# Performance work log

Measured on AMD Instinct MI355X. Metric: run time of the kernel, lower is better.

Reference implementation:

```python
import jax, jax.numpy as jnp
import numpy as np

N_HEAD, D_MODEL, D_K, D_V = 16, 1024, 64, 64
B, L = 8, 1024
LN_EPS = 1e-5
NEG_INF = -1e9


def setup_inputs() -> dict:
    key = jax.random.key(0)
    ks = jax.random.split(key, 12)
    s = 0.02
    return {
        "q": jax.random.normal(ks[0], (B, L, D_MODEL), jnp.float32),
        "k": jax.random.normal(ks[1], (B, L, D_MODEL), jnp.float32),
        "v": jax.random.normal(ks[2], (B, L, D_MODEL), jnp.float32),
        "mask": jnp.zeros((B, L, L), dtype=bool),
        "wq": jax.random.normal(ks[3], (D_MODEL, N_HEAD * D_K), jnp.float32) * s,
        "bq": jnp.zeros((N_HEAD * D_K,), jnp.float32),
        "wk": jax.random.normal(ks[4], (D_MODEL, N_HEAD * D_K), jnp.float32) * s,
        "bk": jnp.zeros((N_HEAD * D_K,), jnp.float32),
        "wv": jax.random.normal(ks[5], (D_MODEL, N_HEAD * D_V), jnp.float32) * s,
        "bv": jnp.zeros((N_HEAD * D_V,), jnp.float32),
        "wo": jax.random.normal(ks[6], (N_HEAD * D_V, D_MODEL), jnp.float32) * s,
        "bo": jnp.zeros((D_MODEL,), jnp.float32),
        "gamma": jnp.ones((D_MODEL,), jnp.float32),
        "beta": jnp.zeros((D_MODEL,), jnp.float32),
    }


def reference(q, k, v, mask, wq, bq, wk, bk, wv, bv, wo, bo, gamma, beta):
    b, lq, _ = q.shape
    lk = k.shape[1]
    residual = q
    # separate Q/K/V projections, split heads: [b, len, h, d]
    qh = (q @ wq + bq).reshape(b, lq, N_HEAD, D_K)
    kh = (k @ wk + bk).reshape(b, lk, N_HEAD, D_K)
    vh = (v @ wv + bv).reshape(b, lk, N_HEAD, D_V)
    # scaled dot-product attention (temperature = sqrt(d_k))
    scores = jnp.einsum("bqhd,bkhd->bhqk", qh, kh) / jnp.sqrt(jnp.float32(D_K))
    scores = jnp.where(mask[:, None, :, :], NEG_INF, scores)
    attn = jax.nn.softmax(scores, axis=-1)  # [b, h, lq, lk]
    ctx = jnp.einsum("bhqk,bkhd->bqhd", attn, vh).reshape(b, lq, N_HEAD * D_V)
    # out-proj (dropout is identity in eval) + residual + LayerNorm
    out = ctx @ wo + bo + residual
    mu = out.mean(-1, keepdims=True)
    var = out.var(-1, keepdims=True)
    out = (out - mu) * jax.lax.rsqrt(var + LN_EPS) * gamma + beta
    # match original attn layout: [n_head*b, lq, lk]
    attn_flat = attn.transpose(1, 0, 2, 3).reshape(N_HEAD * b, lq, lk)
    return out, attn_flat
```

## Files before the change

kernel.cpp:

```cpp
#include <hip/hip_runtime.h>
#include <stdint.h>

static constexpr int BATCH  = 8;
static constexpr int SEQ    = 1024;
static constexpr int DMODEL = 1024;
static constexpr int NHEAD  = 16;

typedef __attribute__((ext_vector_type(8))) short sh8;
typedef __attribute__((ext_vector_type(4))) float fl4;

__device__ __forceinline__ uint16_t f2bf(float f) {
    union { float f; uint32_t u; } a; a.f = f;
    uint32_t r = a.u + 0x7FFFu + ((a.u >> 16) & 1u);
    return (uint16_t)(r >> 16);
}

__device__ __forceinline__ float b2f(uint16_t u) {
    union { uint32_t u; float f; } a; a.u = ((uint32_t)u) << 16; return a.f;
}

__device__ __forceinline__ uint32_t cvtpk(float lo, float hi) {
    uint32_t r;
    asm("v_cvt_pk_bf16_f32 %0, %1, %2" : "=v"(r) : "v"(lo), "v"(hi));
    return r;
}

__device__ __forceinline__ sh8 pack_bf8(fl4 x0, fl4 x1) {
    union { uint32_t w[4]; sh8 v; } pk;
    pk.w[0] = cvtpk(x0[0], x0[1]); pk.w[1] = cvtpk(x0[2], x0[3]);
    pk.w[2] = cvtpk(x1[0], x1[1]); pk.w[3] = cvtpk(x1[2], x1[3]);
    return pk.v;
}

__device__ __forceinline__ fl4 mfma16(sh8 a, sh8 b, fl4 c) {
    return __builtin_amdgcn_mfma_f32_16x16x32_bf16(a, b, c, 0, 0, 0);
}

__device__ __forceinline__ void gload16(const void* g, void* l) {
    __builtin_amdgcn_global_load_lds(
        (const __attribute__((address_space(1))) void*)g,
        (__attribute__((address_space(3))) void*)l, 16, 0, 0);
}

__global__ __launch_bounds__(256) void prep_kernel(const float* __restrict__ wq, const float* __restrict__ wk,
                                                   const float* __restrict__ wv, const float* __restrict__ wo,
                                                   uint16_t* __restrict__ tq, uint16_t* __restrict__ tk,
                                                   uint16_t* __restrict__ tv, uint16_t* __restrict__ to) {
    __shared__ uint16_t T[64][72];
    const int z = blockIdx.z;
    const int tid = threadIdx.x;
    const float* w = (z == 0) ? wq : (z == 1) ? wk : (z == 2) ? wv : wo;
    uint16_t* wT = (z == 0) ? tq : (z == 1) ? tk : (z == 2) ? tv : to;
    const float ws = (z == 0) ? 0.125f : 1.f;
    const int n0 = blockIdx.x * 64, k0 = blockIdx.y * 64;
    #pragma unroll
    for (int it = 0; it < 4; ++it) {
        int g = it * 256 + tid;
        int r = g >> 4, c = (g & 15) * 4;
        fl4 x = *(const fl4*)(w + (size_t)(k0 + r) * DMODEL + n0 + c);
        T[r][c + 0] = f2bf(x[0] * ws); T[r][c + 1] = f2bf(x[1] * ws);
        T[r][c + 2] = f2bf(x[2] * ws); T[r][c + 3] = f2bf(x[3] * ws);
    }
    __syncthreads();
    #pragma unroll
    for (int it = 0; it < 4; ++it) {
        int g = it * 256 + tid;
        int r = g >> 4, c = (g & 15) * 4;
        ushort4 o;
        o.x = T[c + 0][r]; o.y = T[c + 1][r]; o.z = T[c + 2][r]; o.w = T[c + 3][r];
        *(ushort4*)(wT + (size_t)(n0 + r) * DMODEL + k0 + c) = o;
    }
}

__global__ __launch_bounds__(256)
void gemm_proj(const float* __restrict__ q, const float* __restrict__ k, const float* __restrict__ v,
               const uint16_t* __restrict__ B0, const uint16_t* __restrict__ B1, const uint16_t* __restrict__ B2,
               const float* __restrict__ b0, const float* __restrict__ b1, const float* __restrict__ b2,
               uint16_t* __restrict__ qh, uint16_t* __restrict__ kh, uint16_t* __restrict__ vT) {
    __shared__ uint16_t lds[128 * 128];
    uint16_t* Alds = lds;
    uint16_t* Blds = lds + 128 * 64;
    const int z = blockIdx.z;
    const float* Af    = (z == 0) ? q : (z == 1) ? k : v;
    const uint16_t* Bt = (z == 0) ? B0 : (z == 1) ? B1 : B2;
    const float* bias  = (z == 0) ? b0 : (z == 1) ? b1 : b2;
    const float bs     = (z == 0) ? 0.125f : 1.f;
    const int m0 = blockIdx.x * 128, n0 = blockIdx.y * 128;
    const int tid = threadIdx.x, lane = tid & 63, wid = tid >> 6;
    const int wr = (wid >> 1) * 64, wc = (wid & 1) * 64;
    const int fr = lane & 15, fk = (lane >> 4) * 8, frow4 = (lane >> 4) * 4;

    fl4 acc[4][4];
    #pragma unroll
    for (int i = 0; i < 4; ++i)
        #pragma unroll
        for (int j = 0; j < 4; ++j) acc[i][j] = (fl4){0.f, 0.f, 0.f, 0.f};

    for (int kt = 0; kt < 16; ++kt) {
        const int kb = kt * 64;
        #pragma unroll
        for (int it = 0; it < 4; ++it) {
            const int g = it * 256 + tid;
            const int r = g >> 3, c = (g & 7) << 3;
            const float* p = Af + (size_t)(m0 + r) * DMODEL + kb + c;
            fl4 x0 = *(const fl4*)p, x1 = *(const fl4*)(p + 4);
            *(sh8*)&Alds[r * 64 + c] = pack_bf8(x0, x1);
            const int lofs = __builtin_amdgcn_readfirstlane((it * 256 + wid * 64) * 16);
            gload16(Bt + (size_t)(n0 + r) * DMODEL + kb + c, (char*)Blds + lofs);
        }
        __syncthreads();
        #pragma unroll
        for (int ks = 0; ks < 2; ++ks) {
            sh8 a[4], bb[4];
            #pragma unroll
            for (int mi = 0; mi < 4; ++mi) a[mi] = *(const sh8*)&Alds[(wr + mi * 16 + fr) * 64 + ks * 32 + fk];
            #pragma unroll
            for (int ni = 0; ni < 4; ++ni) bb[ni] = *(const sh8*)&Blds[(wc + ni * 16 + fr) * 64 + ks * 32 + fk];
            #pragma unroll
            for (int mi = 0; mi < 4; ++mi)
                #pragma unroll
                for (int ni = 0; ni < 4; ++ni) acc[mi][ni] = mfma16(a[mi], bb[ni], acc[mi][ni]);
        }
        __syncthreads();
    }

    if (z < 2) {
        #pragma unroll
        for (int mi = 0; mi < 4; ++mi) {
            #pragma unroll
            for (int ni = 0; ni < 4; ++ni) {
                const int col = wc + ni * 16 + fr;
                const float bv = bias[n0 + col] * bs;
                #pragma unroll
                for (int i = 0; i < 4; ++i) {
                    const int row = wr + mi * 16 + frow4 + i;
                    lds[row * 128 + ((((col >> 3) ^ (row & 7)) << 3) | (col & 7))] = f2bf(acc[mi][ni][i] + bv);
                }
            }
        }
        __syncthreads();
        uint16_t* Cv = (z == 0) ? qh : kh;
        #pragma unroll
        for (int it = 0; it < 8; ++it) {
            const int ch = it * 256 + tid;
            const int row = ch >> 4, cc = ch & 15;
            sh8 vv = *(sh8*)&lds[row * 128 + ((cc ^ (row & 7)) << 3)];
            *(sh8*)(Cv + (size_t)(m0 + row) * DMODEL + n0 + cc * 8) = vv;
        }
    } else {
        #pragma unroll
        for (int mi = 0; mi < 4; ++mi) {
            #pragma unroll
            for (int ni = 0; ni < 4; ++ni) {
                const int col = wc + ni * 16 + fr;
                const float bv = bias[n0 + col];
                #pragma unroll
                for (int i = 0; i < 4; ++i) {
                    const int row = wr + mi * 16 + frow4 + i;
                    lds[col * 128 + ((((row >> 3) ^ (col & 7)) << 3) | (row & 7))] = f2bf(acc[mi][ni][i] + bv);
                }
            }
        }
        __syncthreads();
        const int b = m0 >> 10, l0 = m0 & 1023;
        #pragma unroll
        for (int it = 0; it < 8; ++it) {
            const int ch = it * 256 + tid;
            const int col = ch >> 4, rc = ch & 15;
            sh8 vv = *(sh8*)&lds[col * 128 + ((rc ^ (col & 7)) << 3)];
            *(sh8*)(vT + (size_t)(b * 1024 + n0 + col) * SEQ + l0 + rc * 8) = vv;
        }
    }
}

__global__ __launch_bounds__(256)
void gemm_out(const uint16_t* __restrict__ Ab, const uint16_t* __restrict__ Bt,
              const float* __restrict__ bias, const float* __restrict__ resid,
              float* __restrict__ Cv) {
    __shared__ uint16_t lds[128 * 128];
    uint16_t* Alds = lds;
    uint16_t* Blds = lds + 128 * 64;
    const int m0 = blockIdx.x * 128, n0 = blockIdx.y * 128;
    const int tid = threadIdx.x, lane = tid & 63, wid = tid >> 6;
    const int wr = (wid >> 1) * 64, wc = (wid & 1) * 64;
    const int fr = lane & 15, fk = (lane >> 4) * 8, frow4 = (lane >> 4) * 4;

    fl4 acc[4][4];
    #pragma unroll
    for (int i = 0; i < 4; ++i)
        #pragma unroll
        for (int j = 0; j < 4; ++j) acc[i][j] = (fl4){0.f, 0.f, 0.f, 0.f};

    for (int kt = 0; kt < 16; ++kt) {
        const int kb = kt * 64;
        #pragma unroll
        for (int it = 0; it < 4; ++it) {
            const int g = it * 256 + tid;
            const int r = g >> 3, c = (g & 7) << 3;
            const int lofs = __builtin_amdgcn_readfirstlane((it * 256 + wid * 64) * 16);
            gload16(Ab + (size_t)(m0 + r) * DMODEL + kb + c, (char*)Alds + lofs);
            gload16(Bt + (size_t)(n0 + r) * DMODEL + kb + c, (char*)Blds + lofs);
        }
        __syncthreads();
        #pragma unroll
        for (int ks = 0; ks < 2; ++ks) {
            sh8 a[4], bb[4];
            #pragma unroll
            for (int mi = 0; mi < 4; ++mi) a[mi] = *(const sh8*)&Alds[(wr + mi * 16 + fr) * 64 + ks * 32 + fk];
            #pragma unroll
            for (int ni = 0; ni < 4; ++ni) bb[ni] = *(const sh8*)&Blds[(wc + ni * 16 + fr) * 64 + ks * 32 + fk];
            #pragma unroll
            for (int mi = 0; mi < 4; ++mi)
                #pragma unroll
                for (int ni = 0; ni < 4; ++ni) acc[mi][ni] = mfma16(a[mi], bb[ni], acc[mi][ni]);
        }
        __syncthreads();
    }

    float* flds = (float*)lds;
    #pragma unroll
    for (int h2 = 0; h2 < 2; ++h2) {
        if (h2) __syncthreads();
        if (wc == h2 * 64) {
            #pragma unroll
            for (int ni = 0; ni < 4; ++ni) {
                const int col = wc + ni * 16 + fr;
                const int ch = col - h2 * 64;
                const float bv = bias[n0 + col];
                #pragma unroll
                for (int mi = 0; mi < 4; ++mi) {
                    #pragma unroll
                    for (int i = 0; i < 4; ++i) {
                        const int row = wr + mi * 16 + frow4 + i;
                        float val = acc[mi][ni][i] + bv;
                        val += resid[(size_t)(m0 + row) * DMODEL + n0 + col];
                        flds[row * 64 + ((((ch >> 2) ^ (row & 7)) << 2) | (ch & 3))] = val;
                    }
                }
            }
        }
        __syncthreads();
        #pragma unroll
        for (int it = 0; it < 8; ++it) {
            const int ck = it * 256 + tid;
            const int row = ck >> 4, cc = ck & 15;
            fl4 vv = *(fl4*)&flds[row * 64 + ((cc ^ (row & 7)) << 2)];
            *(fl4*)(Cv + (size_t)(m0 + row) * DMODEL + n0 + h2 * 64 + cc * 4) = vv;
        }
    }
}

__global__ __launch_bounds__(256)
void attn_kernel(const uint16_t* __restrict__ qh, const uint16_t* __restrict__ kh,
                 const uint16_t* __restrict__ vT, const uint8_t* __restrict__ mask,
                 float* __restrict__ attn, uint16_t* __restrict__ ctx) {
    __shared__ uint16_t S[16 * 1024];
    __shared__ float rinv[16];
    const int b = blockIdx.x, h = blockIdx.y, q0 = blockIdx.z * 16;
    const int tid = threadIdx.x, lane = tid & 63, wid = tid >> 6;
    const int fr = lane & 15, fk = (lane >> 4) * 8, frow4 = (lane >> 4) * 4;

    sh8 Aq[2];
    #pragma unroll
    for (int ks = 0; ks < 2; ++ks)
        Aq[ks] = *(const sh8*)(qh + (size_t)(b * SEQ + q0 + fr) * DMODEL + h * 64 + ks * 32 + fk);

    for (int t8 = 0; t8 < 8; ++t8) {
        const int kv0 = (t8 * 4 + wid) * 32;
        sh8 Bk[2][2];
        #pragma unroll
        for (int ni = 0; ni < 2; ++ni)
            #pragma unroll
            for (int ks = 0; ks < 2; ++ks)
                Bk[ni][ks] = *(const sh8*)(kh + (size_t)(b * SEQ + kv0 + ni * 16 + fr) * DMODEL + h * 64 + ks * 32 + fk);
        fl4 sa[2];
        #pragma unroll
        for (int ni = 0; ni < 2; ++ni) sa[ni] = (fl4){0.f, 0.f, 0.f, 0.f};
        #pragma unroll
        for (int ni = 0; ni < 2; ++ni)
            #pragma unroll
            for (int ks = 0; ks < 2; ++ks) sa[ni] = mfma16(Aq[ks], Bk[ni][ks], sa[ni]);
        #pragma unroll
        for (int ni = 0; ni < 2; ++ni)
            #pragma unroll
            for (int i = 0; i < 4; ++i) {
                const int row = frow4 + i, col = kv0 + ni * 16 + fr;
                S[row * 1024 + ((((col >> 3) ^ (row & 15)) << 3) | (col & 7))] = f2bf(sa[ni][i]);
            }
    }
    __syncthreads();

    {
        const int r = tid >> 4, j = tid & 15;
        const int rbase = r * 1024;
        const uint8_t* mbase = mask + (size_t)(b * SEQ + q0 + r) * SEQ;
        sh8 x[8];
        uint2 mw[8];
        #pragma unroll
        for (int c4 = 0; c4 < 8; ++c4) {
            const int cc = c4 * 16 + j;
            x[c4] = *(sh8*)&S[rbase + ((cc ^ r) << 3)];
            mw[c4] = *(const uint2*)(mbase + cc * 8);
        }
        uint32_t anym = 0;
        #pragma unroll
        for (int c4 = 0; c4 < 8; ++c4) anym |= (mw[c4].x | mw[c4].y);
        float mx = -1e30f;
        if (anym == 0) {
            #pragma unroll
            for (int c4 = 0; c4 < 8; ++c4)
                #pragma unroll
                for (int t = 0; t < 8; ++t) mx = fmaxf(mx, b2f((uint16_t)x[c4][t]));
        } else {
            #pragma unroll
            for (int c4 = 0; c4 < 8; ++c4) {
                float f[8];
                #pragma unroll
                for (int t = 0; t < 4; ++t)
                    f[t] = ((mw[c4].x >> (t * 8)) & 0xFF) ? -1e9f : b2f((uint16_t)x[c4][t]);
                #pragma unroll
                for (int t = 0; t < 4; ++t)
                    f[4 + t] = ((mw[c4].y >> (t * 8)) & 0xFF) ? -1e9f : b2f((uint16_t)x[c4][4 + t]);
                union { uint32_t w[4]; sh8 v; } pk;
                pk.w[0] = cvtpk(f[0], f[1]); pk.w[1] = cvtpk(f[2], f[3]);
                pk.w[2] = cvtpk(f[4], f[5]); pk.w[3] = cvtpk(f[6], f[7]);
                x[c4] = pk.v;
                #pragma unroll
                for (int t = 0; t < 8; ++t) mx = fmaxf(mx, f[t]);
            }
        }
        #pragma unroll
        for (int d = 1; d < 16; d <<= 1) mx = fmaxf(mx, __shfl_xor(mx, d));
        float sum = 0.f;
        #pragma unroll
        for (int c4 = 0; c4 < 8; ++c4) {
            const int cc = c4 * 16 + j;
            float e[8];
            #pragma unroll
            for (int t = 0; t < 8; ++t) e[t] = __expf(b2f((uint16_t)x[c4][t]) - mx);
            union { uint32_t w[4]; sh8 v; } pk;
            pk.w[0] = cvtpk(e[0], e[1]); pk.w[1] = cvtpk(e[2], e[3]);
            pk.w[2] = cvtpk(e[4], e[5]); pk.w[3] = cvtpk(e[6], e[7]);
            *(sh8*)&S[rbase + ((cc ^ r) << 3)] = pk.v;
            sum += e[0] + e[1] + e[2] + e[3] + e[4] + e[5] + e[6] + e[7];
        }
        #pragma unroll
        for (int d = 1; d < 16; d <<= 1) sum += __shfl_xor(sum, d);
        if (j == 0) rinv[r] = 1.f / sum;
    }
    __syncthreads();

    {
        float* ab = attn + ((size_t)((h * BATCH + b) * SEQ + q0)) * SEQ;
        #pragma unroll
        for (int it = 0; it < 16; ++it) {
            const int ch = it * 256 + tid;
            const int row = ch >> 8, oc = ch & 255;
            const int cc = oc >> 1, half = oc & 1;
            const ushort4 p = *(const ushort4*)&S[row * 1024 + ((cc ^ row) << 3) + half * 4];
            const float ri = rinv[row];
            fl4 o;
            o[0] = b2f(p.x) * ri; o[1] = b2f(p.y) * ri;
            o[2] = b2f(p.z) * ri; o[3] = b2f(p.w) * ri;
            __builtin_nontemporal_store(o, (fl4*)(ab + (size_t)ch * 4));
        }
    }

    fl4 acc0 = (fl4){0.f, 0.f, 0.f, 0.f}, acc1 = (fl4){0.f, 0.f, 0.f, 0.f};
    const uint16_t* vbase = vT + (size_t)((b * NHEAD + h) * 64 + wid * 16) * SEQ;
    #pragma unroll 4
    for (int ks2 = 0; ks2 < 32; ++ks2) {
        const int kv = ks2 * 32;
        sh8 Ap = *(const sh8*)&S[fr * 1024 + ((((kv + fk) >> 3) ^ fr) << 3)];
        sh8 Bv = *(const sh8*)(vbase + (size_t)fr * SEQ + kv + fk);
        if (ks2 & 1) acc1 = mfma16(Ap, Bv, acc1);
        else         acc0 = mfma16(Ap, Bv, acc0);
    }
    __syncthreads();

    {
        uint16_t* Sc = S;
        #pragma unroll
        for (int i = 0; i < 4; ++i) {
            const int qr = frow4 + i;
            Sc[qr * 64 + wid * 16 + fr] = f2bf((acc0[i] + acc1[i]) * rinv[qr]);
        }
        __syncthreads();
        const int row = tid >> 4, c4 = (tid & 15) * 4;
        ushort4 vv = *(ushort4*)&Sc[row * 64 + c4];
        *(ushort4*)(ctx + (size_t)(b * SEQ + q0 + row) * DMODEL + h * 64 + c4) = vv;
    }
}

__global__ __launch_bounds__(256)
void ln_kernel(const float* __restrict__ raw, const float* __restrict__ gamma,
               const float* __restrict__ beta, float* __restrict__ out) {
    const int row = blockIdx.x;
    const int tid = threadIdx.x;
    const float* x = raw + (size_t)row * DMODEL;
    fl4 xv = *(const fl4*)(x + tid * 4);
    float s  = xv[0] + xv[1] + xv[2] + xv[3];
    float ss = xv[0] * xv[0] + xv[1] * xv[1] + xv[2] * xv[2] + xv[3] * xv[3];
    #pragma unroll
    for (int d = 1; d < 64; d <<= 1) { s += __shfl_xor(s, d); ss += __shfl_xor(ss, d); }
    __shared__ float sb[4], ssb[4];
    if ((tid & 63) == 0) { sb[tid >> 6] = s; ssb[tid >> 6] = ss; }
    __syncthreads();
    s  = sb[0] + sb[1] + sb[2] + sb[3];
    ss = ssb[0] + ssb[1] + ssb[2] + ssb[3];
    const float mu  = s * (1.f / 1024.f);
    const float var = ss * (1.f / 1024.f) - mu * mu;
    const float rstd = rsqrtf(var + 1e-5f);
    fl4 g  = *(const fl4*)(gamma + tid * 4);
    fl4 be = *(const fl4*)(beta + tid * 4);
    fl4 o;
    #pragma unroll
    for (int j = 0; j < 4; ++j) o[j] = (xv[j] - mu) * rstd * g[j] + be[j];
    *(fl4*)(out + (size_t)row * DMODEL + tid * 4) = o;
}

extern "C" void kernel_launch(void* const* d_in, const int* in_sizes, int n_in,
                              void* d_out, int out_size, void* d_ws, size_t ws_size,
                              hipStream_t stream) {
    (void)in_sizes; (void)n_in; (void)out_size; (void)ws_size;
    const float* q     = (const float*)d_in[0];
    const float* k     = (const float*)d_in[1];
    const float* v     = (const float*)d_in[2];
    const uint8_t* mask = (const uint8_t*)d_in[3];
    const float* wq = (const float*)d_in[4];
    const float* bq = (const float*)d_in[5];
    const float* wk = (const float*)d_in[6];
    const float* bk = (const float*)d_in[7];
    const float* wv = (const float*)d_in[8];
    const float* bv = (const float*)d_in[9];
    const float* wo = (const float*)d_in[10];
    const float* bo = (const float*)d_in[11];
    const float* gamma = (const float*)d_in[12];
    const float* beta  = (const float*)d_in[13];

    float* out  = (float*)d_out;
    float* attn = out + (size_t)BATCH * SEQ * DMODEL;

    char* ws = (char*)d_ws;
    uint16_t* qh   = (uint16_t*)(ws);
    uint16_t* kh   = (uint16_t*)(ws + ((size_t)16 << 20));
    uint16_t* vT   = (uint16_t*)(ws + ((size_t)32 << 20));
    uint16_t* ctx  = (uint16_t*)(ws + ((size_t)48 << 20));
    uint16_t* wqT  = (uint16_t*)(ws + ((size_t)64 << 20));
    uint16_t* wkT  = (uint16_t*)(ws + ((size_t)66 << 20));
    uint16_t* wvT  = (uint16_t*)(ws + ((size_t)68 << 20));
    uint16_t* woT  = (uint16_t*)(ws + ((size_t)70 << 20));

    dim3 tb(256);
    prep_kernel<<<dim3(16, 16, 4), tb, 0, stream>>>(wq, wk, wv, wo, wqT, wkT, wvT, woT);

    gemm_proj<<<dim3(64, 8, 3), tb, 0, stream>>>(q, k, v, wqT, wkT, wvT,
                                                 bq, bk, bv, qh, kh, vT);

    attn_kernel<<<dim3(BATCH, NHEAD, 64), tb, 0, stream>>>(qh, kh, vT, mask, attn, ctx);

    gemm_out<<<dim3(64, 8), tb, 0, stream>>>(ctx, woT, bo, q, out);

    ln_kernel<<<BATCH * SEQ, tb, 0, stream>>>(out, gamma, beta, out);
}
```

Before: 416.7 us.

## Raise wave priority around attention MFMAs and use one wave per LayerNorm row

Measured after the change: 436.0 us. 1.05x slower.

```diff
diff --git a/kernel.cpp b/kernel.cpp
--- a/kernel.cpp
+++ b/kernel.cpp
@@ -276,10 +276,12 @@
         fl4 sa[2];
         #pragma unroll
         for (int ni = 0; ni < 2; ++ni) sa[ni] = (fl4){0.f, 0.f, 0.f, 0.f};
+        __builtin_amdgcn_s_setprio(1);
         #pragma unroll
         for (int ni = 0; ni < 2; ++ni)
             #pragma unroll
             for (int ks = 0; ks < 2; ++ks) sa[ni] = mfma16(Aq[ks], Bk[ni][ks], sa[ni]);
+        __builtin_amdgcn_s_setprio(0);
         #pragma unroll
         for (int ni = 0; ni < 2; ++ni)
             #pragma unroll
@@ -373,8 +375,10 @@
         const int kv = ks2 * 32;
         sh8 Ap = *(const sh8*)&S[fr * 1024 + ((((kv + fk) >> 3) ^ fr) << 3)];
         sh8 Bv = *(const sh8*)(vbase + (size_t)fr * SEQ + kv + fk);
+        __builtin_amdgcn_s_setprio(1);
         if (ks2 & 1) acc1 = mfma16(Ap, Bv, acc1);
         else         acc0 = mfma16(Ap, Bv, acc0);
+        __builtin_amdgcn_s_setprio(0);
     }
     __syncthreads();
 
@@ -395,28 +399,31 @@
 __global__ __launch_bounds__(256)
 void ln_kernel(const float* __restrict__ raw, const float* __restrict__ gamma,
                const float* __restrict__ beta, float* __restrict__ out) {
-    const int row = blockIdx.x;
-    const int tid = threadIdx.x;
+    const int row = blockIdx.x * 4 + (threadIdx.x >> 6);
+    const int lane = threadIdx.x & 63;
     const float* x = raw + (size_t)row * DMODEL;
-    fl4 xv = *(const fl4*)(x + tid * 4);
-    float s  = xv[0] + xv[1] + xv[2] + xv[3];
-    float ss = xv[0] * xv[0] + xv[1] * xv[1] + xv[2] * xv[2] + xv[3] * xv[3];
+    fl4 xv[4];
+    float s = 0.f, ss = 0.f;
+    #pragma unroll
+    for (int i = 0; i < 4; ++i) {
+        xv[i] = *(const fl4*)(x + i * 256 + lane * 4);
+        #pragma unroll
+        for (int j = 0; j < 4; ++j) { s += xv[i][j]; ss += xv[i][j] * xv[i][j]; }
+    }
     #pragma unroll
     for (int d = 1; d < 64; d <<= 1) { s += __shfl_xor(s, d); ss += __shfl_xor(ss, d); }
-    __shared__ float sb[4], ssb[4];
-    if ((tid & 63) == 0) { sb[tid >> 6] = s; ssb[tid >> 6] = ss; }
-    __syncthreads();
-    s  = sb[0] + sb[1] + sb[2] + sb[3];
-    ss = ssb[0] + ssb[1] + ssb[2] + ssb[3];
     const float mu  = s * (1.f / 1024.f);
     const float var = ss * (1.f / 1024.f) - mu * mu;
     const float rstd = rsqrtf(var + 1e-5f);
-    fl4 g  = *(const fl4*)(gamma + tid * 4);
-    fl4 be = *(const fl4*)(beta + tid * 4);
-    fl4 o;
-    #pragma unroll
-    for (int j = 0; j < 4; ++j) o[j] = (xv[j] - mu) * rstd * g[j] + be[j];
-    *(fl4*)(out + (size_t)row * DMODEL + tid * 4) = o;
+    #pragma unroll
+    for (int i = 0; i < 4; ++i) {
+        fl4 g  = *(const fl4*)(gamma + i * 256 + lane * 4);
+        fl4 be = *(const fl4*)(beta  + i * 256 + lane * 4);
+        fl4 o;
+        #pragma unroll
+        for (int j = 0; j < 4; ++j) o[j] = (xv[i][j] - mu) * rstd * g[j] + be[j];
+        __builtin_nontemporal_store(o, (fl4*)(out + (size_t)row * DMODEL + i * 256 + lane * 4));
+    }
 }
 
 extern "C" void kernel_launch(void* const* d_in, const int* in_sizes, int n_in,
@@ -461,5 +468,5 @@
 
     gemm_out<<<dim3(64, 8), tb, 0, stream>>>(ctx, woT, bo, q, out);
 
-    ln_kernel<<<BATCH * SEQ, tb, 0, stream>>>(out, gamma, beta, out);
-}
+    ln_kernel<<<BATCH * SEQ / 4, tb, 0, stream>>>(out, gamma, beta, out);
+}
```
